# Performance work log

Measured on AMD Instinct MI355X. Metric: run time of the kernel, lower is better.

The kernel has to match this reference:

```python
import jax, jax.numpy as jnp
import numpy as np

IN_FEATURES = 1024
OUT_FEATURES = 3072  # out = OUT_FEATURES // 3 = 1024
BATCH = 8192


def _hamilton_block(r, i, j, k):
    # r,i,j,k: (in_features, out) -> (4*in_features, 4*out) quaternion block matrix
    col_r = jnp.concatenate([r, i, j, k], axis=0)
    col_i = jnp.concatenate([i, r, -k, j], axis=0)
    col_j = jnp.concatenate([j, k, r, -i], axis=0)
    col_k = jnp.concatenate([k, -j, i, r], axis=0)
    return jnp.concatenate([col_r, col_i, col_j, col_k], axis=1)


def setup_inputs() -> dict:
    key = jax.random.key(0)
    kx, kr, ki, kj, kk = jax.random.split(key, 5)
    s = 1.0 / np.sqrt(2.0 * (IN_FEATURES + OUT_FEATURES))  # glorot scale
    wshape = (IN_FEATURES, OUT_FEATURES)
    return {
        "x": jax.random.normal(kx, (BATCH, 4 * IN_FEATURES), dtype=jnp.float32),
        "r_weight": s * jax.random.normal(kr, wshape, dtype=jnp.float32),
        "i_weight": s * jax.random.normal(ki, wshape, dtype=jnp.float32),
        "j_weight": s * jax.random.normal(kj, wshape, dtype=jnp.float32),
        "k_weight": s * jax.random.normal(kk, wshape, dtype=jnp.float32),
        "drop": 0,
    }


def reference(x, r_weight, i_weight, j_weight, k_weight, drop):
    out = OUT_FEATURES // 3
    outputs = []
    for c in range(3):  # three gate slices (i, f, a)
        sl = slice(c * out, (c + 1) * out)
        W = _hamilton_block(r_weight[:, sl], i_weight[:, sl],
                            j_weight[:, sl], k_weight[:, sl])
        outputs.append(x @ W)  # (batch, 4*out); bias never added (bug in source: `bias is True`)
    return tuple(outputs)
```

## Files before the change

kernel.cpp:

```cpp
#include <hip/hip_runtime.h>
#include <hip/hip_bf16.h>


typedef __attribute__((ext_vector_type(4))) float        fx4;
typedef __attribute__((ext_vector_type(8))) short        bfx8;
typedef __attribute__((ext_vector_type(4))) float        accx4;
typedef __attribute__((ext_vector_type(4))) unsigned int ux4;

#define WT_ELEMS   (4u * 3072u * 1024u)
#define X_ELEMS    (8192u * 4096u)
#define WS_NEEDED  ((size_t)(WT_ELEMS + X_ELEMS) * 2u)

static __device__ __forceinline__ ushort f2bf(float f) {
  __hip_bfloat16 h = __float2bfloat16(f);
  return *reinterpret_cast<ushort*>(&h);
}

static __device__ __forceinline__ void gload16(const ushort* g, ushort* l) {
  __builtin_amdgcn_global_load_lds(
      (const __attribute__((address_space(1))) unsigned int*)g,
      (__attribute__((address_space(3))) unsigned int*)l, 16, 0, 0);
}

__global__ __launch_bounds__(256) void conv_x(const float* __restrict__ x,
                                              ushort* __restrict__ xb) {
  const int total = (int)(X_ELEMS / 8u);
  for (int i = blockIdx.x * 256 + threadIdx.x; i < total; i += gridDim.x * 256) {
    fx4 a = *reinterpret_cast<const fx4*>(x + (size_t)i * 8);
    fx4 b = *reinterpret_cast<const fx4*>(x + (size_t)i * 8 + 4);
    bfx8 o;
    #pragma unroll
    for (int j = 0; j < 4; ++j) {
      o[j]     = (short)f2bf(a[j]);
      o[4 + j] = (short)f2bf(b[j]);
    }
    *reinterpret_cast<bfx8*>(xb + (size_t)i * 8) = o;
  }
}

__global__ __launch_bounds__(256) void conv_w(const float* __restrict__ w0,
                                              const float* __restrict__ w1,
                                              const float* __restrict__ w2,
                                              const float* __restrict__ w3,
                                              ushort* __restrict__ wt) {
  __shared__ ushort T[64][65];
  const float* w = (blockIdx.z == 0) ? w0 : (blockIdx.z == 1) ? w1
                 : (blockIdx.z == 2) ? w2 : w3;
  ushort* dst = wt + (size_t)blockIdx.z * 3072u * 1024u;
  const int n0 = blockIdx.x * 64;
  const int k0 = blockIdx.y * 64;
  const int tid = threadIdx.x;

  const int rcol = tid & 63, rrow = tid >> 6;
  #pragma unroll
  for (int i = 0; i < 16; ++i) {
    int r = i * 4 + rrow;
    T[r][rcol] = f2bf(w[(size_t)(k0 + r) * 3072 + n0 + rcol]);
  }
  __syncthreads();

  const int wc = (tid & 15) * 4, wr = tid >> 4;
  #pragma unroll
  for (int i = 0; i < 4; ++i) {
    int r = i * 16 + wr;
    ushort4 v;
    v.x = T[wc + 0][r]; v.y = T[wc + 1][r];
    v.z = T[wc + 2][r]; v.w = T[wc + 3][r];
    *reinterpret_cast<ushort4*>(dst + (size_t)(n0 + r) * 1024 + k0 + wc) = v;
  }
}

__global__ __launch_bounds__(256) void qgemm(const ushort* __restrict__ wt,
                                             const ushort* __restrict__ xb,
                                             float* __restrict__ out) {
  __shared__ __align__(16) ushort As[128 * 32];
  __shared__ __align__(16) ushort Bs[128 * 32];

  const int flat = blockIdx.x;
  const int swz  = (flat & 7) * 768 + (flat >> 3);
  const int by = swz / 96, bx = swz % 96;
  const int m0 = by * 128, n0 = bx * 128;

  const int gate = n0 >> 12;
  const int rem  = n0 & 4095;
  const int qc   = rem >> 10;
  const int nb   = gate * 1024 + (rem & 1023);

  const int tid = threadIdx.x, lane = tid & 63, wid = tid >> 6;
  const int wm = (wid >> 1) * 64, wn = (wid & 1) * 64;
  const int l15 = lane & 15, l16 = lane >> 4;

  const int srow = wid * 16 + (lane >> 2);
  const int scol = (lane & 3) * 8;
  const ushort* aP = xb + (size_t)(m0 + srow) * 4096 + scol;
  const ushort* bP = wt + (size_t)(nb + srow) * 1024 + scol;
  ushort* aL = As + wid * 16 * 32;
  ushort* bL = Bs + wid * 16 * 32;

  accx4 acc[4][4];
  #pragma unroll
  for (int i = 0; i < 4; ++i)
    #pragma unroll
    for (int j = 0; j < 4; ++j)
      acc[i][j] = (accx4){0.f, 0.f, 0.f, 0.f};

  for (int t = 0; t < 128; ++t) {
    const int qr   = t >> 5;
    const int comp = qc ^ qr;
    const int k1   = (t * 32) & 1023;
    const bool neg = (qc == 1 && qr == 2) || (qc == 2 && qr == 3) || (qc == 3 && qr == 1);
    const ushort* aPt = aP + t * 32;
    const ushort* bPt = bP + (size_t)comp * 3072u * 1024u + k1;

    __syncthreads();
    gload16(aPt,              aL);
    gload16(aPt + 64 * 4096,  aL + 64 * 32);
    gload16(bPt,              bL);
    gload16(bPt + 64 * 1024,  bL + 64 * 32);
    __syncthreads();

    bfx8 af[4];
    ux4  bu[4];
    #pragma unroll
    for (int f = 0; f < 4; ++f) {
      af[f] = *reinterpret_cast<const bfx8*>(As + (wm + f * 16 + l15) * 32 + l16 * 8);
      bu[f] = *reinterpret_cast<const ux4*>(Bs + (wn + f * 16 + l15) * 32 + l16 * 8);
    }
    if (neg) {
      #pragma unroll
      for (int f = 0; f < 4; ++f) bu[f] ^= 0x80008000u;
    }
    union { ux4 u; bfx8 h; } bc[4];
    #pragma unroll
    for (int f = 0; f < 4; ++f) bc[f].u = bu[f];

    #pragma unroll
    for (int i = 0; i < 4; ++i)
      #pragma unroll
      for (int j = 0; j < 4; ++j)
        acc[i][j] = __builtin_amdgcn_mfma_f32_16x16x32_bf16(af[i], bc[j].h, acc[i][j], 0, 0, 0);
  }

  const size_t gatebase = (size_t)gate * (8192ull * 4096ull);
  #pragma unroll
  for (int i = 0; i < 4; ++i) {
    #pragma unroll
    for (int j = 0; j < 4; ++j) {
      const int ncol = rem + wn + j * 16 + l15;
      #pragma unroll
      for (int r = 0; r < 4; ++r) {
        const int mrow = m0 + wm + i * 16 + (l16 << 2) + r;
        out[gatebase + (size_t)mrow * 4096 + ncol] = acc[i][j][r];
      }
    }
  }
}

__global__ __launch_bounds__(256) void qlin_fallback(
    const float* __restrict__ x,
    const float* __restrict__ wr_, const float* __restrict__ wi_,
    const float* __restrict__ wj_, const float* __restrict__ wk_,
    float* __restrict__ out)
{
  __shared__ __align__(16) ushort As[128][32];
  __shared__ __align__(16) ushort Bs[128][32];
  const int tid = threadIdx.x;
  const int n0  = blockIdx.x * 128;
  const int m0  = blockIdx.y * 128;
  const int gate = n0 >> 12, rem = n0 & 4095, qc = rem >> 10;
  const int colbase = gate * 1024 + (rem & 1023);
  const int arow = tid >> 1, acol = (tid & 1) << 4;
  const float* aptr = x + (size_t)(m0 + arow) * 4096 + acol;
  const int bng = (tid & 31) << 2, bkg = (tid >> 5) << 2;
  const int lane = tid & 63, wid = tid >> 6;
  const int wm = (wid >> 1) * 64, wn = (wid & 1) * 64;
  const int l15 = lane & 15, l16 = lane >> 4;
  accx4 acc[4][4];
  #pragma unroll
  for (int i = 0; i < 4; ++i)
    #pragma unroll
    for (int j = 0; j < 4; ++j) acc[i][j] = (accx4){0.f,0.f,0.f,0.f};

  for (int t = 0; t < 128; ++t) {
    const int qr = t >> 5, ci = qc ^ qr;
    const float* wsel = (ci==0)?wr_:(ci==1)?wi_:(ci==2)?wj_:wk_;
    const bool neg = (qc==1&&qr==2)||(qc==2&&qr==3)||(qc==3&&qr==1);
    const float sgn = neg ? -1.f : 1.f;
    __syncthreads();
    {
      const float* ap = aptr + t * 32;
      fx4 av0 = *reinterpret_cast<const fx4*>(ap);
      fx4 av1 = *reinterpret_cast<const fx4*>(ap + 4);
      fx4 av2 = *reinterpret_cast<const fx4*>(ap + 8);
      fx4 av3 = *reinterpret_cast<const fx4*>(ap + 12);
      bfx8 p0, p1;
      #pragma unroll
      for (int j = 0; j < 4; ++j) {
        p0[j] = (short)f2bf(av0[j]); p0[4+j] = (short)f2bf(av1[j]);
        p1[j] = (short)f2bf(av2[j]); p1[4+j] = (short)f2bf(av3[j]);
      }
      *reinterpret_cast<bfx8*>(&As[arow][acol])     = p0;
      *reinterpret_cast<bfx8*>(&As[arow][acol + 8]) = p1;
      const float* bp = wsel + (size_t)((t & 31) * 32 + bkg) * 3072 + colbase + bng;
      #pragma unroll
      for (int j = 0; j < 4; ++j) {
        fx4 bv = *reinterpret_cast<const fx4*>(bp + (size_t)j * 3072);
        ushort4 cw;
        cw.x = f2bf(bv[0]*sgn); cw.y = f2bf(bv[1]*sgn);
        cw.z = f2bf(bv[2]*sgn); cw.w = f2bf(bv[3]*sgn);
        *reinterpret_cast<ushort4*>(&Bs[bng + j][bkg]) = cw;
      }
    }
    __syncthreads();
    bfx8 af[4], bfr[4];
    #pragma unroll
    for (int f = 0; f < 4; ++f) {
      af[f]  = *reinterpret_cast<const bfx8*>(&As[wm + f*16 + l15][l16*8]);
      bfr[f] = *reinterpret_cast<const bfx8*>(&Bs[wn + f*16 + l15][l16*8]);
    }
    #pragma unroll
    for (int i = 0; i < 4; ++i)
      #pragma unroll
      for (int j = 0; j < 4; ++j)
        acc[i][j] = __builtin_amdgcn_mfma_f32_16x16x32_bf16(af[i], bfr[j], acc[i][j], 0, 0, 0);
  }
  const size_t gatebase = (size_t)gate * (8192ull * 4096ull);
  #pragma unroll
  for (int i = 0; i < 4; ++i)
    #pragma unroll
    for (int j = 0; j < 4; ++j) {
      const int ncol = rem + wn + j * 16 + l15;
      #pragma unroll
      for (int r = 0; r < 4; ++r) {
        const int mrow = m0 + wm + i * 16 + (l16 << 2) + r;
        out[gatebase + (size_t)mrow * 4096 + ncol] = acc[i][j][r];
      }
    }
}

extern "C" void kernel_launch(void* const* d_in, const int* in_sizes, int n_in,
                              void* d_out, int out_size, void* d_ws, size_t ws_size,
                              hipStream_t stream) {
  const float* x  = (const float*)d_in[0];
  const float* wr = (const float*)d_in[1];
  const float* wi = (const float*)d_in[2];
  const float* wj = (const float*)d_in[3];
  const float* wk = (const float*)d_in[4];
  float* out = (float*)d_out;

  if (ws_size >= WS_NEEDED) {
    ushort* wt = (ushort*)d_ws;
    ushort* xb = wt + WT_ELEMS;
    conv_x<<<4096, 256, 0, stream>>>(x, xb);
    dim3 gw(48, 16, 4);
    conv_w<<<gw, 256, 0, stream>>>(wr, wi, wj, wk, wt);
    qgemm<<<6144, 256, 0, stream>>>(wt, xb, out);
  } else {
    dim3 grid(96, 64);
    qlin_fallback<<<grid, 256, 0, stream>>>(x, wr, wi, wj, wk, out);
  }
}
```

Before: 1.497 ms.

## Enlarge qgemm tiles to 256x256 with 4-stage LDS pipeline and swizzled layout

```diff
diff --git a/kernel.cpp b/kernel.cpp
--- a/kernel.cpp
+++ b/kernel.cpp
@@ -70,16 +70,15 @@
   }
 }
 
-__global__ __launch_bounds__(256) void qgemm(const ushort* __restrict__ wt,
-                                             const ushort* __restrict__ xb,
-                                             float* __restrict__ out) {
-  __shared__ __align__(16) ushort As[128 * 32];
-  __shared__ __align__(16) ushort Bs[128 * 32];
+__global__ __launch_bounds__(512, 2) void qgemm(const ushort* __restrict__ wt,
+                                                const ushort* __restrict__ xb,
+                                                float* __restrict__ out) {
+  __shared__ __align__(16) ushort lds[65536];
 
   const int flat = blockIdx.x;
-  const int swz  = (flat & 7) * 768 + (flat >> 3);
-  const int by = swz / 96, bx = swz % 96;
-  const int m0 = by * 128, n0 = bx * 128;
+  const int swzb = (flat & 7) * 192 + (flat >> 3);
+  const int by = swzb / 48, bx = swzb % 48;
+  const int m0 = by * 256, n0 = bx * 256;
 
   const int gate = n0 >> 12;
   const int rem  = n0 & 4095;
@@ -87,70 +86,97 @@
   const int nb   = gate * 1024 + (rem & 1023);
 
   const int tid = threadIdx.x, lane = tid & 63, wid = tid >> 6;
-  const int wm = (wid >> 1) * 64, wn = (wid & 1) * 64;
+  const int wr = wid >> 2, wc = wid & 3;
   const int l15 = lane & 15, l16 = lane >> 4;
 
-  const int srow = wid * 16 + (lane >> 2);
-  const int scol = (lane & 3) * 8;
-  const ushort* aP = xb + (size_t)(m0 + srow) * 4096 + scol;
-  const ushort* bP = wt + (size_t)(nb + srow) * 1024 + scol;
-  ushort* aL = As + wid * 16 * 32;
-  ushort* bL = Bs + wid * 16 * 32;
-
-  accx4 acc[4][4];
-  #pragma unroll
-  for (int i = 0; i < 4; ++i)
+  const int srow = tid >> 2;
+  const int sg   = ((tid & 3) - (srow >> 1)) & 3;
+  const ushort* aG0 = xb + (size_t)(m0 + srow) * 4096 + sg * 8;
+  const ushort* bG0 = wt + (size_t)(nb + srow) * 1024 + sg * 8;
+  const int aLo = wid * 512;
+  const int bLo = 8192 + wid * 512;
+
+  accx4 acc[8][4];
+  #pragma unroll
+  for (int f = 0; f < 8; ++f)
     #pragma unroll
     for (int j = 0; j < 4; ++j)
-      acc[i][j] = (accx4){0.f, 0.f, 0.f, 0.f};
+      acc[f][j] = (accx4){0.f, 0.f, 0.f, 0.f};
+
+  auto stage = [&](int kt) {
+    const int buf  = (kt & 3) * 16384;
+    const int comp = qc ^ (kt >> 5);
+    const ushort* aS = aG0 + kt * 32;
+    const ushort* bS = bG0 + (size_t)comp * 3145728u + ((kt * 32) & 1023);
+    gload16(aS,              lds + buf + aLo);
+    gload16(aS + 128 * 4096, lds + buf + aLo + 4096);
+    gload16(bS,              lds + buf + bLo);
+    gload16(bS + 128 * 1024, lds + buf + bLo + 4096);
+  };
+
+  stage(0); stage(1); stage(2);
+  asm volatile("s_waitcnt vmcnt(8)" ::: "memory");
+  __builtin_amdgcn_sched_barrier(0);
+  __builtin_amdgcn_s_barrier();
+  __builtin_amdgcn_sched_barrier(0);
 
   for (int t = 0; t < 128; ++t) {
-    const int qr   = t >> 5;
-    const int comp = qc ^ qr;
-    const int k1   = (t * 32) & 1023;
+    const int buf = (t & 3) * 16384;
+    const int qr  = t >> 5;
     const bool neg = (qc == 1 && qr == 2) || (qc == 2 && qr == 3) || (qc == 3 && qr == 1);
-    const ushort* aPt = aP + t * 32;
-    const ushort* bPt = bP + (size_t)comp * 3072u * 1024u + k1;
-
-    __syncthreads();
-    gload16(aPt,              aL);
-    gload16(aPt + 64 * 4096,  aL + 64 * 32);
-    gload16(bPt,              bL);
-    gload16(bPt + 64 * 1024,  bL + 64 * 32);
-    __syncthreads();
-
-    bfx8 af[4];
+
+    bfx8 af[8];
     ux4  bu[4];
     #pragma unroll
-    for (int f = 0; f < 4; ++f) {
-      af[f] = *reinterpret_cast<const bfx8*>(As + (wm + f * 16 + l15) * 32 + l16 * 8);
-      bu[f] = *reinterpret_cast<const ux4*>(Bs + (wn + f * 16 + l15) * 32 + l16 * 8);
+    for (int f = 0; f < 8; ++f) {
+      const int row  = wr * 128 + f * 16 + l15;
+      const int slot = (l16 + (row >> 1)) & 3;
+      af[f] = *reinterpret_cast<const bfx8*>(lds + buf + row * 32 + slot * 8);
+    }
+    #pragma unroll
+    for (int j = 0; j < 4; ++j) {
+      const int row  = wc * 64 + j * 16 + l15;
+      const int slot = (l16 + (row >> 1)) & 3;
+      bu[j] = *reinterpret_cast<const ux4*>(lds + buf + 8192 + row * 32 + slot * 8);
     }
     if (neg) {
       #pragma unroll
-      for (int f = 0; f < 4; ++f) bu[f] ^= 0x80008000u;
+      for (int j = 0; j < 4; ++j) bu[j] ^= 0x80008000u;
     }
     union { ux4 u; bfx8 h; } bc[4];
     #pragma unroll
-    for (int f = 0; f < 4; ++f) bc[f].u = bu[f];
-
-    #pragma unroll
-    for (int i = 0; i < 4; ++i)
+    for (int j = 0; j < 4; ++j) bc[j].u = bu[j];
+
+    if (t < 125) stage(t + 3);
+
+    __builtin_amdgcn_s_setprio(1);
+    #pragma unroll
+    for (int f = 0; f < 8; ++f)
       #pragma unroll
       for (int j = 0; j < 4; ++j)
-        acc[i][j] = __builtin_amdgcn_mfma_f32_16x16x32_bf16(af[i], bc[j].h, acc[i][j], 0, 0, 0);
+        acc[f][j] = __builtin_amdgcn_mfma_f32_16x16x32_bf16(af[f], bc[j].h, acc[f][j], 0, 0, 0);
+    __builtin_amdgcn_s_setprio(0);
+
+    if (t < 125)       { asm volatile("s_waitcnt vmcnt(8)" ::: "memory"); }
+    else if (t == 125) { asm volatile("s_waitcnt vmcnt(4)" ::: "memory"); }
+    else if (t == 126) { asm volatile("s_waitcnt vmcnt(0)" ::: "memory"); }
+    if (t < 127) {
+      __builtin_amdgcn_sched_barrier(0);
+      __builtin_amdgcn_s_barrier();
+      __builtin_amdgcn_sched_barrier(0);
+    }
   }
 
   const size_t gatebase = (size_t)gate * (8192ull * 4096ull);
   #pragma unroll
-  for (int i = 0; i < 4; ++i) {
-    #pragma unroll
-    for (int j = 0; j < 4; ++j) {
-      const int ncol = rem + wn + j * 16 + l15;
+  for (int f = 0; f < 8; ++f) {
+    #pragma unroll
+    for (int j = 0; j < 4; ++j) {
+      const int ncol = rem + wc * 64 + j * 16 + l15;
       #pragma unroll
       for (int r = 0; r < 4; ++r) {
-        const int mrow = m0 + wm + i * 16 + (l16 << 2) + r;
-        out[gatebase + (size_t)mrow * 4096 + ncol] = acc[i][j][r];
+        const int mrow = m0 + wr * 128 + f * 16 + (l16 << 2) + r;
+        out[gatebase + (size_t)mrow * 4096 + ncol] = acc[f][j][r];
       }
     }
   }
@@ -254,7 +280,7 @@
     conv_x<<<4096, 256, 0, stream>>>(x, xb);
     dim3 gw(48, 16, 4);
     conv_w<<<gw, 256, 0, stream>>>(wr, wi, wj, wk, wt);
-    qgemm<<<6144, 256, 0, stream>>>(wt, xb, out);
+    qgemm<<<1536, 512, 0, stream>>>(wt, xb, out);
   } else {
     dim3 grid(96, 64);
     qlin_fallback<<<grid, 256, 0, stream>>>(x, wr, wi, wj, wk, out);
```

Measured after the change: 1.217 ms. -18.7%, faster.
